# Kernel tuning notes

Hardware: AMD Instinct MI355X
Metric: run time of the kernel (lower is better)

The kernel has to match this reference:

```python
import jax, jax.numpy as jnp
import numpy as np

N = 50000      # nodes (both x and t sets)
D = 128        # d_hidden
E = 1600000    # edges per edge_index (avg degree 32)
LN_EPS = 1e-5


def _gin(x_src, x_dst, edge, W1, b1, W2, b2):
    # PyG GINConv, eps=0: nn(x_dst + sum_{j->i} x_src[j])
    agg = jax.ops.segment_sum(x_src[edge[0]], edge[1], num_segments=x_dst.shape[0])
    h = x_dst + agg
    h = jax.nn.relu(h @ W1 + b1)
    return h @ W2 + b2


def _layernorm(h, g, b):
    m = jnp.mean(h, axis=-1, keepdims=True)
    v = jnp.var(h, axis=-1, keepdims=True)
    return (h - m) / jnp.sqrt(v + LN_EPS) * g + b


def setup_inputs() -> dict:
    key = jax.random.key(0)
    ks = jax.random.split(key, 24)
    s = 1.0 / np.sqrt(D)
    w = lambda k: (jax.random.uniform(k, (D, D), dtype=jnp.float32) * 2 - 1) * s
    b = lambda k: (jax.random.uniform(k, (D,), dtype=jnp.float32) * 2 - 1) * s
    return {
        "x": jax.random.normal(ks[0], (N, D), dtype=jnp.float32),
        "t": jax.random.normal(ks[1], (N, D), dtype=jnp.float32),
        "e_t": jax.random.randint(ks[2], (2, E), 0, N),
        "e_xct": jax.random.randint(ks[3], (2, E), 0, N),
        # gat_tt GIN MLP
        "W1a": w(ks[4]), "b1a": b(ks[5]), "W2a": w(ks[6]), "b2a": b(ks[7]),
        # gat_xct GIN MLP
        "W1b": w(ks[8]), "b1b": b(ks[9]), "W2b": w(ks[10]), "b2b": b(ks[11]),
        # out: Linear -> ReLU -> LayerNorm
        "Wo": w(ks[12]), "bo": b(ks[13]),
        "ln_g": jnp.ones((D,), dtype=jnp.float32),
        "ln_b": jnp.zeros((D,), dtype=jnp.float32),
        # fc_x: Linear -> ReLU -> Linear
        "Wf1": w(ks[14]), "bf1": b(ks[15]), "Wf2": w(ks[16]), "bf2": b(ks[17]),
    }


def reference(x, t, e_t, e_xct,
              W1a, b1a, W2a, b2a,
              W1b, b1b, W2b, b2b,
              Wo, bo, ln_g, ln_b,
              Wf1, bf1, Wf2, bf2):
    # t = (t + gat_tt(t, e_t) + gat_xct((x, t), e_xct)).relu()
    t2 = jax.nn.relu(t
                     + _gin(t, t, e_t, W1a, b1a, W2a, b2a)
                     + _gin(x, t, e_xct, W1b, b1b, W2b, b2b))
    # out branch: Linear -> ReLU -> LayerNorm, residual add
    t_out = t2 + _layernorm(jax.nn.relu(t2 @ Wo + bo), ln_g, ln_b)
    # fc_x branch: Linear -> ReLU -> Linear, residual add
    x_out = x + (jax.nn.relu(x @ Wf1 + bf1) @ Wf2 + bf2)
    return (x_out, t_out)
```

## Files before the change

kernel.cpp:

```cpp
#include <hip/hip_runtime.h>

#define DD 128
#define BSH 7
#define LSTR 136

typedef __attribute__((ext_vector_type(8))) short bf16x8;
typedef __attribute__((ext_vector_type(4))) float f32x4;
typedef __attribute__((ext_vector_type(2))) float f32x2;

__device__ __forceinline__ unsigned short f2b(float f){
  unsigned u = __builtin_bit_cast(unsigned, f);
  u += 0x7FFFu + ((u >> 16) & 1u);
  return (unsigned short)(u >> 16);
}
__device__ __forceinline__ float blo(unsigned u){ return __builtin_bit_cast(float, u << 16); }
__device__ __forceinline__ float bhi(unsigned u){ return __builtin_bit_cast(float, u & 0xFFFF0000u); }
__device__ __forceinline__ float b2f(unsigned short h){ return __builtin_bit_cast(float, ((unsigned)h) << 16); }
__device__ __forceinline__ unsigned pk2(float a, float b){
  return (unsigned)f2b(a) | ((unsigned)f2b(b) << 16);
}

struct WP { const float* w[7]; };
__global__ __launch_bounds__(256) void k_pre(const float* __restrict__ x,
    const float* __restrict__ t, unsigned* __restrict__ xh, unsigned* __restrict__ th,
    int M, WP p, unsigned short* __restrict__ wt,
    const int* __restrict__ e_t, const int* __restrict__ e_xct,
    int* __restrict__ gbcount, int E, int NBper, int ncv, int N){
  const int bid = blockIdx.x;
  if (bid < ncv){
    int tid = bid*256 + threadIdx.x;
    if (tid < M){
      float4 v = ((const float4*)x)[tid];
      ((uint2*)xh)[tid] = make_uint2(pk2(v.x, v.y), pk2(v.z, v.w));
    } else if (tid < 2*M){
      int k = tid - M;
      float4 v = ((const float4*)t)[k];
      ((uint2*)th)[k] = make_uint2(pk2(v.x, v.y), pk2(v.z, v.w));
    }
    return;
  }
  if (bid < ncv + 7){
    const float* W = p.w[bid - ncv];
    unsigned short* dst = wt + (size_t)(bid - ncv)*DD*DD;
    for (int e = threadIdx.x; e < DD*DD; e += 256){
      int k = e >> 7, c = e & 127;
      dst[(c*DD + k) ^ ((c & 7) << 3)] = f2b(W[e]);
    }
    return;
  }
  if (bid == ncv + 7){
    const int tid = threadIdx.x;
    uint4 z; z.x = 0; z.y = 0; z.z = 0; z.w = 0;
    if (tid < 16)      ((uint4*)(xh + (size_t)N*(DD/2)))[tid]      = z;
    else if (tid < 32) ((uint4*)(th + (size_t)N*(DD/2)))[tid - 16] = z;
    return;
  }
  __shared__ int h[800];
  const int vb = bid - ncv - 8;
  const int NB2 = 2*NBper;
  for (int i = threadIdx.x; i < NB2; i += 256) h[i] = 0;
  __syncthreads();
  const long total = 2L*E;
  for (long idx = (long)vb*256 + threadIdx.x; idx < total; idx += 65536L){
    int s = idx >= E;
    int e = (int)(idx - (s ? (long)E : 0));
    int d = (s ? e_xct : e_t)[E + e];
    atomicAdd(&h[s*NBper + (d >> BSH)], 1);
  }
  __syncthreads();
  for (int i = threadIdx.x; i < NB2; i += 256)
    if (h[i]) atomicAdd(&gbcount[i], h[i]);
}

__global__ void k_bscan(const int* __restrict__ gbcount, int* __restrict__ gbase,
                        int* __restrict__ gcursor, int NB2, int total){
  __shared__ int sm[1024];
  const int t = threadIdx.x;
  int v = (t < NB2) ? gbcount[t] : 0;
  sm[t] = v; __syncthreads();
  for (int d = 1; d < 1024; d <<= 1){
    int u = (t >= d) ? sm[t-d] : 0;
    __syncthreads();
    sm[t] += u;
    __syncthreads();
  }
  if (t < NB2){ int ex = sm[t] - v; gbase[t] = ex; gcursor[t] = ex; }
  if (t == 0) gbase[NB2] = total;
}

#define SCCH 8192
__global__ __launch_bounds__(256) void k_scatter(const int* __restrict__ e_t,
    const int* __restrict__ e_xct, int* __restrict__ gcursor,
    unsigned* __restrict__ gbucket, int E, int NBper){
  __shared__ int cnt[800]; __shared__ int gpos[800]; __shared__ int cur[800];
  const int NB2 = 2*NBper;
  const int t = threadIdx.x;
  for (int i = t; i < NB2; i += 256){ cnt[i] = 0; cur[i] = 0; }
  __syncthreads();
  const long base = (long)blockIdx.x * SCCH;
  const long end  = min(base + SCCH, 2L*E);
  for (long idx = base + t; idx < end; idx += 256){
    int s = idx >= E;
    int e = (int)(idx - (s ? (long)E : 0));
    int d = (s ? e_xct : e_t)[E + e];
    atomicAdd(&cnt[s*NBper + (d >> BSH)], 1);
  }
  __syncthreads();
  for (int i = t; i < NB2; i += 256)
    if (cnt[i]) gpos[i] = atomicAdd(&gcursor[i], cnt[i]);
  __syncthreads();
  for (long idx = base + t; idx < end; idx += 256){
    int s = idx >= E;
    int e = (int)(idx - (s ? (long)E : 0));
    const int* ei = s ? e_xct : e_t;
    int sv = ei[e];
    int d  = ei[E + e];
    int b  = s*NBper + (d >> BSH);
    int pos = atomicAdd(&cur[b], 1);
    gbucket[gpos[b] + pos] = (unsigned)sv | ((unsigned)d << 16);
  }
}

__global__ __launch_bounds__(256) void k_build(const unsigned* __restrict__ gbucket,
    const int* __restrict__ gbase, int* __restrict__ offs,
    unsigned short* __restrict__ csr, int N, int E, int NBper){
  __shared__ int cnt[128]; __shared__ int pre[128]; __shared__ int cur[128];
  const int b  = blockIdx.x;
  const int s  = b >= NBper;
  const int bb = b - s*NBper;
  const int d0 = bb << BSH;
  const int t  = threadIdx.x;
  if (t < 128) cnt[t] = 0;
  __syncthreads();
  const int g0 = gbase[b], g1 = gbase[b+1];
  for (int j = g0 + t; j < g1; j += 256){
    unsigned en = gbucket[j];
    atomicAdd(&cnt[(en >> 16) & 127], 1);
  }
  __syncthreads();
  int v = (t < 128) ? cnt[t] : 0;
  if (t < 128) pre[t] = v;
  __syncthreads();
  for (int d = 1; d < 128; d <<= 1){
    int u = (t >= d && t < 128) ? pre[t-d] : 0;
    __syncthreads();
    if (t < 128) pre[t] += u;
    __syncthreads();
  }
  if (t < 128){
    int ex = pre[t] - v;
    cur[t] = ex;
    int dd = d0 + t;
    if (dd < N) offs[(size_t)s*(N+1) + dd] = (g0 - s*E) + ex;
  }
  if (t == 128 + 0 && bb == NBper-1) offs[(size_t)s*(N+1) + N] = E;
  __syncthreads();
  for (int j = g0 + t; j < g1; j += 256){
    unsigned en = gbucket[j];
    int d7 = (en >> 16) & 127;
    int pos = atomicAdd(&cur[d7], 1);
    csr[(size_t)g0 + pos] = (unsigned short)(en & 0xFFFFu);
  }
}

__device__ __forceinline__ void gemm_reg(const bf16x8 a[4], int c0, int g, int swz,
    const unsigned short* wimg, f32x4 acc[8]){
  #pragma unroll
  for (int kb = 0; kb < 4; ++kb){
    const int co = (kb*32 + g*8) ^ swz;
    #pragma unroll
    for (int cb = 0; cb < 8; ++cb){
      bf16x8 b = *(const bf16x8*)(wimg + (size_t)(cb*16 + c0)*DD + co);
      acc[cb] = __builtin_amdgcn_mfma_f32_16x16x32_bf16(a[kb], b, acc[cb], 0, 0, 0);
    }
  }
}

__device__ __forceinline__ void gemm_lds(const unsigned short* lds,
    int w, int c0, int g, int swz, const unsigned short* wimg, f32x4 acc[8]){
  const unsigned short* ap = lds + (w*16 + c0)*LSTR + g*8;
  #pragma unroll
  for (int kb = 0; kb < 4; ++kb){
    bf16x8 a = *(const bf16x8*)(ap + kb*32);
    const int co = (kb*32 + g*8) ^ swz;
    #pragma unroll
    for (int cb = 0; cb < 8; ++cb){
      bf16x8 b = *(const bf16x8*)(wimg + (size_t)(cb*16 + c0)*DD + co);
      acc[cb] = __builtin_amdgcn_mfma_f32_16x16x32_bf16(a, b, acc[cb], 0, 0, 0);
    }
  }
}

__global__ __launch_bounds__(256, 4) void k_gather(const unsigned short* __restrict__ th,
    const unsigned short* __restrict__ xh, const int* __restrict__ offs,
    const unsigned short* __restrict__ csr, unsigned short* hA, unsigned short* hB,
    const unsigned short* __restrict__ wt,
    const float* __restrict__ bf1, const float* __restrict__ bf2,
    float* __restrict__ outX,
    int N, int E, int gg){
  __shared__ unsigned short lds[64*LSTR];
  if (blockIdx.x < (unsigned)gg){
    const int bid = blockIdx.x;
    const int tid = threadIdx.x;
    const int w = tid >> 6, l = tid & 63;
    const int g = l >> 4, c0 = l & 15;
    const int swz = (c0 & 7) << 3;
    const int rbase = bid*64 + w*16;
    const unsigned short* Wf1 = wt + 5*DD*DD;
    const unsigned short* Wf2 = wt + 6*DD*DD;

    int arow = rbase + c0; if (arow > N-1) arow = N-1;
    const unsigned short* apX = xh + (size_t)arow*DD + g*8;
    bf16x8 aX[4];
    #pragma unroll
    for (int kb = 0; kb < 4; ++kb) aX[kb] = *(const bf16x8*)(apX + kb*32);
    unsigned short rs_[8][4];
    #pragma unroll
    for (int cb = 0; cb < 8; ++cb){
      #pragma unroll
      for (int r = 0; r < 4; ++r){
        int orow = rbase + 4*g + r;
        int rc = orow > N-1 ? N-1 : orow;
        rs_[cb][r] = xh[(size_t)rc*DD + cb*16 + c0];
      }
    }

    f32x4 acc[8];
    #pragma unroll
    for (int cb = 0; cb < 8; ++cb) acc[cb] = 0.f;
    gemm_reg(aX, c0, g, swz, Wf1, acc);

    #pragma unroll
    for (int cb = 0; cb < 8; ++cb){
      float bv = bf1[cb*16 + c0];
      #pragma unroll
      for (int r = 0; r < 4; ++r)
        lds[(w*16 + 4*g + r)*LSTR + cb*16 + c0] = f2b(fmaxf(acc[cb][r] + bv, 0.f));
    }
    __syncthreads();

    #pragma unroll
    for (int cb = 0; cb < 8; ++cb) acc[cb] = 0.f;
    gemm_lds(lds, w, c0, g, swz, Wf2, acc);

    #pragma unroll
    for (int cb = 0; cb < 8; ++cb){
      float bv = bf2[cb*16 + c0];
      #pragma unroll
      for (int r = 0; r < 4; ++r){
        int orow = rbase + 4*g + r;
        if (orow < N){
          size_t oi = (size_t)orow*DD + cb*16 + c0;
          outX[oi] = acc[cb][r] + bv + b2f(rs_[cb][r]);
        }
      }
    }
    return;
  }
  const int w = threadIdx.x >> 6, l = threadIdx.x & 63;
  const long wid = (long)(blockIdx.x - gg)*4 + w;
  if (wid >= 2L*N) return;
  const int s = wid >= N;
  const int i = (int)(wid - (s ? N : 0));
  const int* off = offs + (size_t)s*(N+1);
  const unsigned short* src = s ? xh : th;
  const unsigned short* cs = csr + (size_t)s*E;
  const int o0 = off[i], o1 = off[i+1];
  const int deg = o1 - o0;
  const int rs = l >> 4;
  const int q  = l & 15;
  const unsigned short* srcq = src + q*8;
  f32x2 A0 = 0.f, A1 = 0.f, A2 = 0.f, A3 = 0.f;
  if (deg > 0){
    int ce = cs[o0 + (l < deg ? l : deg-1)];
    for (int base = 0; base < deg; base += 64){
      const int nb = min(64, deg - base);
      const int ce_cur = ce;
      const int nxt = base + 64;
      if (nxt < deg){
        const int rem2 = deg - nxt;
        ce = cs[o0 + nxt + (l < rem2 ? l : rem2-1)];
      }
      for (int jj = 0; jj < nb; jj += 16){
        #pragma unroll
        for (int u4 = 0; u4 < 4; ++u4){
          const int idx = jj + u4*4 + rs;
          int r = __shfl(ce_cur, idx);
          r = (idx < nb) ? r : N;
          uint4 v = *(const uint4*)(srcq + (size_t)r*DD);
          A0 += (f32x2){blo(v.x), bhi(v.x)};
          A1 += (f32x2){blo(v.y), bhi(v.y)};
          A2 += (f32x2){blo(v.z), bhi(v.z)};
          A3 += (f32x2){blo(v.w), bhi(v.w)};
        }
      }
    }
  }
  #pragma unroll
  for (int m = 16; m <= 32; m <<= 1){
    A0.x += __shfl_xor(A0.x, m); A0.y += __shfl_xor(A0.y, m);
    A1.x += __shfl_xor(A1.x, m); A1.y += __shfl_xor(A1.y, m);
    A2.x += __shfl_xor(A2.x, m); A2.y += __shfl_xor(A2.y, m);
    A3.x += __shfl_xor(A3.x, m); A3.y += __shfl_xor(A3.y, m);
  }
  if (l < 16){
    uint4 tv = *(const uint4*)(th + (size_t)i*DD + q*8);
    A0 += (f32x2){blo(tv.x), bhi(tv.x)};
    A1 += (f32x2){blo(tv.y), bhi(tv.y)};
    A2 += (f32x2){blo(tv.z), bhi(tv.z)};
    A3 += (f32x2){blo(tv.w), bhi(tv.w)};
    uint4 o;
    o.x = pk2(A0.x, A0.y); o.y = pk2(A1.x, A1.y);
    o.z = pk2(A2.x, A2.y); o.w = pk2(A3.x, A3.y);
    *(uint4*)((s ? hB : hA) + (size_t)i*DD + q*8) = o;
  }
}

__device__ __forceinline__ void stage_issue(const unsigned short* __restrict__ Wt,
                                            unsigned short* wlds){
  const int tid = threadIdx.x;
  const int w = tid >> 6, l = tid & 63;
  #pragma unroll
  for (int i = 0; i < 8; ++i){
    const int cbase = i*256 + w*64;
    __builtin_amdgcn_global_load_lds(
      (const __attribute__((address_space(1))) unsigned*)(Wt + (size_t)(cbase + l)*8),
      (__attribute__((address_space(3))) unsigned*)(wlds + (size_t)cbase*8),
      16, 0, 0);
  }
}

__global__ __launch_bounds__(256, 3) void k_tail(
    const unsigned short* __restrict__ hA, const unsigned short* __restrict__ hB,
    const unsigned short* __restrict__ th,
    const unsigned short* __restrict__ wt,
    const float* __restrict__ b1a, const float* __restrict__ b2a,
    const float* __restrict__ b1b, const float* __restrict__ b2b,
    const float* __restrict__ bo,  const float* __restrict__ lng,
    const float* __restrict__ lnb,
    float* __restrict__ outT, int N)
{
  __shared__ unsigned short lds[64*LSTR];
  __shared__ unsigned short wlds[DD*DD];
  const unsigned short* W1a = wt + 0*DD*DD;
  const unsigned short* W2a = wt + 1*DD*DD;
  const unsigned short* W1b = wt + 2*DD*DD;
  const unsigned short* W2b = wt + 3*DD*DD;
  const unsigned short* Wo  = wt + 4*DD*DD;

  const int bid = blockIdx.x;
  const int tid = threadIdx.x;
  const int w = tid >> 6, l = tid & 63;
  const int g = l >> 4, c0 = l & 15;
  const int swz = (c0 & 7) << 3;
  const int rbase = bid*64 + w*16;

  int arow = rbase + c0; if (arow > N-1) arow = N-1;
  const unsigned short* apA = hA + (size_t)arow*DD + g*8;
  const unsigned short* apB = hB + (size_t)arow*DD + g*8;
  bf16x8 aA[4], aB[4];
  #pragma unroll
  for (int kb = 0; kb < 4; ++kb){
    aA[kb] = *(const bf16x8*)(apA + kb*32);
    aB[kb] = *(const bf16x8*)(apB + kb*32);
  }
  unsigned short thr_[8][4];
  #pragma unroll
  for (int cb = 0; cb < 8; ++cb){
    #pragma unroll
    for (int r = 0; r < 4; ++r){
      int orow = rbase + 4*g + r;
      int rc = orow > N-1 ? N-1 : orow;
      thr_[cb][r] = th[(size_t)rc*DD + cb*16 + c0];
    }
  }
  stage_issue(W1a, wlds);
  __syncthreads();

  f32x4 acc[8];

  #pragma unroll
  for (int cb = 0; cb < 8; ++cb) acc[cb] = 0.f;
  gemm_reg(aA, c0, g, swz, wlds, acc);
  __syncthreads();
  stage_issue(W2a, wlds);
  #pragma unroll
  for (int cb = 0; cb < 8; ++cb){
    float bv = b1a[cb*16 + c0];
    #pragma unroll
    for (int r = 0; r < 4; ++r)
      lds[(w*16 + 4*g + r)*LSTR + cb*16 + c0] = f2b(fmaxf(acc[cb][r] + bv, 0.f));
  }
  __syncthreads();

  #pragma unroll
  for (int cb = 0; cb < 8; ++cb) acc[cb] = 0.f;
  gemm_lds(lds, w, c0, g, swz, wlds, acc);
  float pAv[8][4];
  #pragma unroll
  for (int cb = 0; cb < 8; ++cb){
    float bv = b2a[cb*16 + c0];
    #pragma unroll
    for (int r = 0; r < 4; ++r) pAv[cb][r] = acc[cb][r] + bv;
  }
  __syncthreads();
  stage_issue(W1b, wlds);
  __syncthreads();

  #pragma unroll
  for (int cb = 0; cb < 8; ++cb) acc[cb] = 0.f;
  gemm_reg(aB, c0, g, swz, wlds, acc);
  __syncthreads();
  stage_issue(W2b, wlds);
  #pragma unroll
  for (int cb = 0; cb < 8; ++cb){
    float bv = b1b[cb*16 + c0];
    #pragma unroll
    for (int r = 0; r < 4; ++r)
      lds[(w*16 + 4*g + r)*LSTR + cb*16 + c0] = f2b(fmaxf(acc[cb][r] + bv, 0.f));
  }
  __syncthreads();

  #pragma unroll
  for (int cb = 0; cb < 8; ++cb) acc[cb] = 0.f;
  gemm_lds(lds, w, c0, g, swz, wlds, acc);
  __syncthreads();
  stage_issue(Wo, wlds);

  float t2f[8][4];
  #pragma unroll
  for (int cb = 0; cb < 8; ++cb){
    float bv = b2b[cb*16 + c0];
    #pragma unroll
    for (int r = 0; r < 4; ++r){
      float v = fmaxf(acc[cb][r] + bv + b2f(thr_[cb][r]) + pAv[cb][r], 0.f);
      t2f[cb][r] = v;
      lds[(w*16 + 4*g + r)*LSTR + cb*16 + c0] = f2b(v);
    }
  }
  __syncthreads();

  #pragma unroll
  for (int cb = 0; cb < 8; ++cb) acc[cb] = 0.f;
  gemm_lds(lds, w, c0, g, swz, wlds, acc);

  float u[8][4];
  float sm_[4] = {0,0,0,0}, sq_[4] = {0,0,0,0};
  #pragma unroll
  for (int cb = 0; cb < 8; ++cb){
    float bv = bo[cb*16 + c0];
    #pragma unroll
    for (int r = 0; r < 4; ++r){
      float v = fmaxf(acc[cb][r] + bv, 0.f);
      u[cb][r] = v;
      sm_[r] += v; sq_[r] += v*v;
    }
  }
  #pragma unroll
  for (int m = 1; m < 16; m <<= 1){
    #pragma unroll
    for (int r = 0; r < 4; ++r){
      sm_[r] += __shfl_xor(sm_[r], m, 64);
      sq_[r] += __shfl_xor(sq_[r], m, 64);
    }
  }
  float mean[4], rstd[4];
  #pragma unroll
  for (int r = 0; r < 4; ++r){
    mean[r] = sm_[r] * (1.0f/DD);
    float var = sq_[r] * (1.0f/DD) - mean[r]*mean[r];
    rstd[r] = rsqrtf(var + 1e-5f);
  }
  #pragma unroll
  for (int cb = 0; cb < 8; ++cb){
    float gv = lng[cb*16 + c0], bv2 = lnb[cb*16 + c0];
    #pragma unroll
    for (int r = 0; r < 4; ++r){
      int orow = rbase + 4*g + r;
      if (orow < N){
        size_t oi = (size_t)orow*DD + cb*16 + c0;
        outT[oi] = (u[cb][r] - mean[r]) * rstd[r] * gv + bv2 + t2f[cb][r];
      }
    }
  }
}

extern "C" void kernel_launch(void* const* d_in, const int* in_sizes, int n_in,
                              void* d_out, int out_size, void* d_ws, size_t ws_size,
                              hipStream_t stream) {
  const float* x     = (const float*)d_in[0];
  const float* t     = (const float*)d_in[1];
  const int*   e_t   = (const int*)d_in[2];
  const int*   e_xct = (const int*)d_in[3];
  const float* b1a = (const float*)d_in[5];
  const float* b2a = (const float*)d_in[7];
  const float* b1b = (const float*)d_in[9];
  const float* b2b = (const float*)d_in[11];
  const float* bo  = (const float*)d_in[13];
  const float* lng = (const float*)d_in[14];
  const float* lnb = (const float*)d_in[15];
  const float* bf1 = (const float*)d_in[17];
  const float* bf2 = (const float*)d_in[19];

  const int N = in_sizes[0] / DD;
  const int E = in_sizes[2] / 2;
  const int NBper = (N + 127) >> BSH;
  const int NB2 = 2*NBper;

  char* p = (char*)d_ws;
  auto carve = [&](size_t b)->char*{ char* r = p; p += (b + 255) & ~(size_t)255; return r; };
  size_t nd2z = (size_t)(N+1)*DD*2;
  size_t nd2 = (size_t)N*DD*2, nd4 = (size_t)N*DD*4;
  unsigned short* xh = (unsigned short*)carve(nd2z);
  unsigned short* th = (unsigned short*)carve(nd2z);
  unsigned short* hA = (unsigned short*)carve(nd2);
  unsigned short* hB = (unsigned short*)carve(nd2);
  float*          pA = (float*)carve(nd4);
  unsigned short* wt = (unsigned short*)carve((size_t)7*DD*DD*2);
  int* gbcount = (int*)carve((size_t)NB2*4);
  int* gbase   = (int*)carve((size_t)(NB2+1)*4);
  int* gcursor = (int*)carve((size_t)NB2*4);
  int* offs    = (int*)carve((size_t)2*(N+1)*4);
  unsigned short* csr = (unsigned short*)carve((size_t)2*E*2);
  unsigned* gbucket = (unsigned*)pA;

  float* outX = (float*)d_out;
  float* outT = outX + (size_t)N*DD;

  hipMemsetAsync(gbcount, 0, (size_t)NB2*4, stream);

  WP wp;
  wp.w[0] = (const float*)d_in[4];  wp.w[1] = (const float*)d_in[6];
  wp.w[2] = (const float*)d_in[8];  wp.w[3] = (const float*)d_in[10];
  wp.w[4] = (const float*)d_in[12]; wp.w[5] = (const float*)d_in[16];
  wp.w[6] = (const float*)d_in[18];

  const int M4 = N*DD/4;
  const int ncv = (2*M4 + 255)/256;
  k_pre<<<ncv + 8 + 256, 256, 0, stream>>>(x, t, (unsigned*)xh, (unsigned*)th, M4,
                                           wp, wt, e_t, e_xct, gbcount, E, NBper, ncv, N);
  k_bscan<<<1, 1024, 0, stream>>>(gbcount, gbase, gcursor, NB2, 2*E);
  const int nsc = (int)((2L*E + SCCH-1) / SCCH);
  k_scatter<<<nsc, 256, 0, stream>>>(e_t, e_xct, gcursor, gbucket, E, NBper);
  k_build<<<NB2, 256, 0, stream>>>(gbucket, gbase, offs, csr, N, E, NBper);

  const int gg = (N + 63)/64;
  const int ngb = (2*N + 3)/4;
  k_gather<<<gg + ngb, 256, 0, stream>>>(th, xh, offs, csr, hA, hB,
                                         wt, bf1, bf2, outX, N, E, gg);

  k_tail<<<gg, 256, 0, stream>>>(hA, hB, th, wt, b1a, b2a, b1b, b2b, bo,
                                 lng, lnb, outT, N);
}
```

Measured before the change: 254.2 us.

## Move fc_x MLP into scatter kernel, stage weights in LDS, widen tail blocks

Moves the independent x-branch MLP blocks out of the gather kernel and into the edge scatter kernel, so that work runs alongside the memory-bound scatter instead of the gather. The x-branch now stages its weights into LDS with global_load_lds rather than reading them straight from global memory. The tail kernel goes from 256 to 512 threads and handles 128 rows per block, so each staged weight matrix is shared by twice as many rows. The costs are higher LDS use per block, which may limit occupancy of both the scatter and tail kernels, and a less regular mix of work inside the fused kernel.

```diff
diff --git a/kernel.cpp b/kernel.cpp
--- a/kernel.cpp
+++ b/kernel.cpp
@@ -88,36 +88,160 @@
   if (t == 0) gbase[NB2] = total;
 }
 
+__device__ __forceinline__ void gemm_reg(const bf16x8 a[4], int c0, int g, int swz,
+    const unsigned short* wlds, f32x4 acc[8]){
+  #pragma unroll
+  for (int kb = 0; kb < 4; ++kb){
+    const int co = (kb*32 + g*8) ^ swz;
+    #pragma unroll
+    for (int cb = 0; cb < 8; ++cb){
+      bf16x8 b = *(const bf16x8*)(wlds + (cb*16 + c0)*DD + co);
+      acc[cb] = __builtin_amdgcn_mfma_f32_16x16x32_bf16(a[kb], b, acc[cb], 0, 0, 0);
+    }
+  }
+}
+
+__device__ __forceinline__ void gemm_lds(const unsigned short* lds,
+    int w, int c0, int g, int swz, const unsigned short* wlds, f32x4 acc[8]){
+  const unsigned short* ap = lds + (w*16 + c0)*LSTR + g*8;
+  #pragma unroll
+  for (int kb = 0; kb < 4; ++kb){
+    bf16x8 a = *(const bf16x8*)(ap + kb*32);
+    const int co = (kb*32 + g*8) ^ swz;
+    #pragma unroll
+    for (int cb = 0; cb < 8; ++cb){
+      bf16x8 b = *(const bf16x8*)(wlds + (cb*16 + c0)*DD + co);
+      acc[cb] = __builtin_amdgcn_mfma_f32_16x16x32_bf16(a, b, acc[cb], 0, 0, 0);
+    }
+  }
+}
+
+__device__ __forceinline__ void stage_issue_256(const unsigned short* __restrict__ Wt,
+                                                unsigned short* wlds){
+  const int tid = threadIdx.x;
+  const int w = tid >> 6, l = tid & 63;
+  #pragma unroll
+  for (int i = 0; i < 8; ++i){
+    const int cbase = i*256 + w*64;
+    __builtin_amdgcn_global_load_lds(
+      (const __attribute__((address_space(1))) unsigned*)(Wt + (size_t)(cbase + l)*8),
+      (__attribute__((address_space(3))) unsigned*)(wlds + (size_t)cbase*8),
+      16, 0, 0);
+  }
+}
+__device__ __forceinline__ void stage_issue_512(const unsigned short* __restrict__ Wt,
+                                                unsigned short* wlds){
+  const int tid = threadIdx.x;
+  const int w = tid >> 6, l = tid & 63;
+  #pragma unroll
+  for (int i = 0; i < 4; ++i){
+    const int cbase = i*512 + w*64;
+    __builtin_amdgcn_global_load_lds(
+      (const __attribute__((address_space(1))) unsigned*)(Wt + (size_t)(cbase + l)*8),
+      (__attribute__((address_space(3))) unsigned*)(wlds + (size_t)cbase*8),
+      16, 0, 0);
+  }
+}
+
 #define SCCH 8192
-__global__ __launch_bounds__(256) void k_scatter(const int* __restrict__ e_t,
+__global__ __launch_bounds__(256, 3) void k_scatmlp(const int* __restrict__ e_t,
     const int* __restrict__ e_xct, int* __restrict__ gcursor,
-    unsigned* __restrict__ gbucket, int E, int NBper){
-  __shared__ int cnt[800]; __shared__ int gpos[800]; __shared__ int cur[800];
-  const int NB2 = 2*NBper;
-  const int t = threadIdx.x;
-  for (int i = t; i < NB2; i += 256){ cnt[i] = 0; cur[i] = 0; }
-  __syncthreads();
-  const long base = (long)blockIdx.x * SCCH;
-  const long end  = min(base + SCCH, 2L*E);
-  for (long idx = base + t; idx < end; idx += 256){
-    int s = idx >= E;
-    int e = (int)(idx - (s ? (long)E : 0));
-    int d = (s ? e_xct : e_t)[E + e];
-    atomicAdd(&cnt[s*NBper + (d >> BSH)], 1);
-  }
-  __syncthreads();
-  for (int i = t; i < NB2; i += 256)
-    if (cnt[i]) gpos[i] = atomicAdd(&gcursor[i], cnt[i]);
-  __syncthreads();
-  for (long idx = base + t; idx < end; idx += 256){
-    int s = idx >= E;
-    int e = (int)(idx - (s ? (long)E : 0));
-    const int* ei = s ? e_xct : e_t;
-    int sv = ei[e];
-    int d  = ei[E + e];
-    int b  = s*NBper + (d >> BSH);
-    int pos = atomicAdd(&cur[b], 1);
-    gbucket[gpos[b] + pos] = (unsigned)sv | ((unsigned)d << 16);
+    unsigned* __restrict__ gbucket, int E, int NBper, int nsc,
+    const unsigned short* __restrict__ xh, const unsigned short* __restrict__ wt,
+    const float* __restrict__ bf1, const float* __restrict__ bf2,
+    float* __restrict__ outX, int N){
+  __shared__ __align__(16) unsigned char smem[50176];
+  if (blockIdx.x < (unsigned)nsc){
+    int* cnt  = (int*)smem;
+    int* gpos = cnt + 800;
+    int* cur  = gpos + 800;
+    const int NB2 = 2*NBper;
+    const int t = threadIdx.x;
+    for (int i = t; i < NB2; i += 256){ cnt[i] = 0; cur[i] = 0; }
+    __syncthreads();
+    const long base = (long)blockIdx.x * SCCH;
+    const long end  = min(base + SCCH, 2L*E);
+    for (long idx = base + t; idx < end; idx += 256){
+      int s = idx >= E;
+      int e = (int)(idx - (s ? (long)E : 0));
+      int d = (s ? e_xct : e_t)[E + e];
+      atomicAdd(&cnt[s*NBper + (d >> BSH)], 1);
+    }
+    __syncthreads();
+    for (int i = t; i < NB2; i += 256)
+      if (cnt[i]) gpos[i] = atomicAdd(&gcursor[i], cnt[i]);
+    __syncthreads();
+    for (long idx = base + t; idx < end; idx += 256){
+      int s = idx >= E;
+      int e = (int)(idx - (s ? (long)E : 0));
+      const int* ei = s ? e_xct : e_t;
+      int sv = ei[e];
+      int d  = ei[E + e];
+      int b  = s*NBper + (d >> BSH);
+      int pos = atomicAdd(&cur[b], 1);
+      gbucket[gpos[b] + pos] = (unsigned)sv | ((unsigned)d << 16);
+    }
+    return;
+  }
+  unsigned short* lds  = (unsigned short*)smem;
+  unsigned short* wlds = (unsigned short*)(smem + 17408);
+  const unsigned short* Wf1 = wt + 5*DD*DD;
+  const unsigned short* Wf2 = wt + 6*DD*DD;
+  const int bid = blockIdx.x - nsc;
+  const int tid = threadIdx.x;
+  const int w = tid >> 6, l = tid & 63;
+  const int g = l >> 4, c0 = l & 15;
+  const int swz = (c0 & 7) << 3;
+  const int rbase = bid*64 + w*16;
+
+  int arow = rbase + c0; if (arow > N-1) arow = N-1;
+  const unsigned short* apX = xh + (size_t)arow*DD + g*8;
+  bf16x8 aX[4];
+  #pragma unroll
+  for (int kb = 0; kb < 4; ++kb) aX[kb] = *(const bf16x8*)(apX + kb*32);
+  unsigned short rs_[8][4];
+  #pragma unroll
+  for (int cb = 0; cb < 8; ++cb){
+    #pragma unroll
+    for (int r = 0; r < 4; ++r){
+      int orow = rbase + 4*g + r;
+      int rc = orow > N-1 ? N-1 : orow;
+      rs_[cb][r] = xh[(size_t)rc*DD + cb*16 + c0];
+    }
+  }
+  stage_issue_256(Wf1, wlds);
+  __syncthreads();
+
+  f32x4 acc[8];
+  #pragma unroll
+  for (int cb = 0; cb < 8; ++cb) acc[cb] = 0.f;
+  gemm_reg(aX, c0, g, swz, wlds, acc);
+  __syncthreads();
+  stage_issue_256(Wf2, wlds);
+  #pragma unroll
+  for (int cb = 0; cb < 8; ++cb){
+    float bv = bf1[cb*16 + c0];
+    #pragma unroll
+    for (int r = 0; r < 4; ++r)
+      lds[(w*16 + 4*g + r)*LSTR + cb*16 + c0] = f2b(fmaxf(acc[cb][r] + bv, 0.f));
+  }
+  __syncthreads();
+
+  #pragma unroll
+  for (int cb = 0; cb < 8; ++cb) acc[cb] = 0.f;
+  gemm_lds(lds, w, c0, g, swz, wlds, acc);
+
+  #pragma unroll
+  for (int cb = 0; cb < 8; ++cb){
+    float bv = bf2[cb*16 + c0];
+    #pragma unroll
+    for (int r = 0; r < 4; ++r){
+      int orow = rbase + 4*g + r;
+      if (orow < N){
+        size_t oi = (size_t)orow*DD + cb*16 + c0;
+        outX[oi] = acc[cb][r] + bv + b2f(rs_[cb][r]);
+      }
+    }
   }
 }
 
@@ -163,102 +287,12 @@
   }
 }
 
-__device__ __forceinline__ void gemm_reg(const bf16x8 a[4], int c0, int g, int swz,
-    const unsigned short* wimg, f32x4 acc[8]){
-  #pragma unroll
-  for (int kb = 0; kb < 4; ++kb){
-    const int co = (kb*32 + g*8) ^ swz;
-    #pragma unroll
-    for (int cb = 0; cb < 8; ++cb){
-      bf16x8 b = *(const bf16x8*)(wimg + (size_t)(cb*16 + c0)*DD + co);
-      acc[cb] = __builtin_amdgcn_mfma_f32_16x16x32_bf16(a[kb], b, acc[cb], 0, 0, 0);
-    }
-  }
-}
-
-__device__ __forceinline__ void gemm_lds(const unsigned short* lds,
-    int w, int c0, int g, int swz, const unsigned short* wimg, f32x4 acc[8]){
-  const unsigned short* ap = lds + (w*16 + c0)*LSTR + g*8;
-  #pragma unroll
-  for (int kb = 0; kb < 4; ++kb){
-    bf16x8 a = *(const bf16x8*)(ap + kb*32);
-    const int co = (kb*32 + g*8) ^ swz;
-    #pragma unroll
-    for (int cb = 0; cb < 8; ++cb){
-      bf16x8 b = *(const bf16x8*)(wimg + (size_t)(cb*16 + c0)*DD + co);
-      acc[cb] = __builtin_amdgcn_mfma_f32_16x16x32_bf16(a, b, acc[cb], 0, 0, 0);
-    }
-  }
-}
-
-__global__ __launch_bounds__(256, 4) void k_gather(const unsigned short* __restrict__ th,
+__global__ __launch_bounds__(256) void k_gather(const unsigned short* __restrict__ th,
     const unsigned short* __restrict__ xh, const int* __restrict__ offs,
     const unsigned short* __restrict__ csr, unsigned short* hA, unsigned short* hB,
-    const unsigned short* __restrict__ wt,
-    const float* __restrict__ bf1, const float* __restrict__ bf2,
-    float* __restrict__ outX,
-    int N, int E, int gg){
-  __shared__ unsigned short lds[64*LSTR];
-  if (blockIdx.x < (unsigned)gg){
-    const int bid = blockIdx.x;
-    const int tid = threadIdx.x;
-    const int w = tid >> 6, l = tid & 63;
-    const int g = l >> 4, c0 = l & 15;
-    const int swz = (c0 & 7) << 3;
-    const int rbase = bid*64 + w*16;
-    const unsigned short* Wf1 = wt + 5*DD*DD;
-    const unsigned short* Wf2 = wt + 6*DD*DD;
-
-    int arow = rbase + c0; if (arow > N-1) arow = N-1;
-    const unsigned short* apX = xh + (size_t)arow*DD + g*8;
-    bf16x8 aX[4];
-    #pragma unroll
-    for (int kb = 0; kb < 4; ++kb) aX[kb] = *(const bf16x8*)(apX + kb*32);
-    unsigned short rs_[8][4];
-    #pragma unroll
-    for (int cb = 0; cb < 8; ++cb){
-      #pragma unroll
-      for (int r = 0; r < 4; ++r){
-        int orow = rbase + 4*g + r;
-        int rc = orow > N-1 ? N-1 : orow;
-        rs_[cb][r] = xh[(size_t)rc*DD + cb*16 + c0];
-      }
-    }
-
-    f32x4 acc[8];
-    #pragma unroll
-    for (int cb = 0; cb < 8; ++cb) acc[cb] = 0.f;
-    gemm_reg(aX, c0, g, swz, Wf1, acc);
-
-    #pragma unroll
-    for (int cb = 0; cb < 8; ++cb){
-      float bv = bf1[cb*16 + c0];
-      #pragma unroll
-      for (int r = 0; r < 4; ++r)
-        lds[(w*16 + 4*g + r)*LSTR + cb*16 + c0] = f2b(fmaxf(acc[cb][r] + bv, 0.f));
-    }
-    __syncthreads();
-
-    #pragma unroll
-    for (int cb = 0; cb < 8; ++cb) acc[cb] = 0.f;
-    gemm_lds(lds, w, c0, g, swz, Wf2, acc);
-
-    #pragma unroll
-    for (int cb = 0; cb < 8; ++cb){
-      float bv = bf2[cb*16 + c0];
-      #pragma unroll
-      for (int r = 0; r < 4; ++r){
-        int orow = rbase + 4*g + r;
-        if (orow < N){
-          size_t oi = (size_t)orow*DD + cb*16 + c0;
-          outX[oi] = acc[cb][r] + bv + b2f(rs_[cb][r]);
-        }
-      }
-    }
-    return;
-  }
+    int N, int E){
   const int w = threadIdx.x >> 6, l = threadIdx.x & 63;
-  const long wid = (long)(blockIdx.x - gg)*4 + w;
+  const long wid = (long)blockIdx.x*4 + w;
   if (wid >= 2L*N) return;
   const int s = wid >= N;
   const int i = (int)(wid - (s ? N : 0));
@@ -316,21 +350,7 @@
   }
 }
 
-__device__ __forceinline__ void stage_issue(const unsigned short* __restrict__ Wt,
-                                            unsigned short* wlds){
-  const int tid = threadIdx.x;
-  const int w = tid >> 6, l = tid & 63;
-  #pragma unroll
-  for (int i = 0; i < 8; ++i){
-    const int cbase = i*256 + w*64;
-    __builtin_amdgcn_global_load_lds(
-      (const __attribute__((address_space(1))) unsigned*)(Wt + (size_t)(cbase + l)*8),
-      (__attribute__((address_space(3))) unsigned*)(wlds + (size_t)cbase*8),
-      16, 0, 0);
-  }
-}
-
-__global__ __launch_bounds__(256, 3) void k_tail(
+__global__ __launch_bounds__(512, 4) void k_tail(
     const unsigned short* __restrict__ hA, const unsigned short* __restrict__ hB,
     const unsigned short* __restrict__ th,
     const unsigned short* __restrict__ wt,
@@ -340,7 +360,7 @@
     const float* __restrict__ lnb,
     float* __restrict__ outT, int N)
 {
-  __shared__ unsigned short lds[64*LSTR];
+  __shared__ unsigned short lds[128*LSTR];
   __shared__ unsigned short wlds[DD*DD];
   const unsigned short* W1a = wt + 0*DD*DD;
   const unsigned short* W2a = wt + 1*DD*DD;
@@ -353,7 +373,7 @@
   const int w = tid >> 6, l = tid & 63;
   const int g = l >> 4, c0 = l & 15;
   const int swz = (c0 & 7) << 3;
-  const int rbase = bid*64 + w*16;
+  const int rbase = bid*128 + w*16;
 
   int arow = rbase + c0; if (arow > N-1) arow = N-1;
   const unsigned short* apA = hA + (size_t)arow*DD + g*8;
@@ -374,7 +394,7 @@
       thr_[cb][r] = th[(size_t)rc*DD + cb*16 + c0];
     }
   }
-  stage_issue(W1a, wlds);
+  stage_issue_512(W1a, wlds);
   __syncthreads();
 
   f32x4 acc[8];
@@ -383,7 +403,7 @@
   for (int cb = 0; cb < 8; ++cb) acc[cb] = 0.f;
   gemm_reg(aA, c0, g, swz, wlds, acc);
   __syncthreads();
-  stage_issue(W2a, wlds);
+  stage_issue_512(W2a, wlds);
   #pragma unroll
   for (int cb = 0; cb < 8; ++cb){
     float bv = b1a[cb*16 + c0];
@@ -404,14 +424,14 @@
     for (int r = 0; r < 4; ++r) pAv[cb][r] = acc[cb][r] + bv;
   }
   __syncthreads();
-  stage_issue(W1b, wlds);
+  stage_issue_512(W1b, wlds);
   __syncthreads();
 
   #pragma unroll
   for (int cb = 0; cb < 8; ++cb) acc[cb] = 0.f;
   gemm_reg(aB, c0, g, swz, wlds, acc);
   __syncthreads();
-  stage_issue(W2b, wlds);
+  stage_issue_512(W2b, wlds);
   #pragma unroll
   for (int cb = 0; cb < 8; ++cb){
     float bv = b1b[cb*16 + c0];
@@ -425,7 +445,7 @@
   for (int cb = 0; cb < 8; ++cb) acc[cb] = 0.f;
   gemm_lds(lds, w, c0, g, swz, wlds, acc);
   __syncthreads();
-  stage_issue(Wo, wlds);
+  stage_issue_512(Wo, wlds);
 
   float t2f[8][4];
   #pragma unroll
@@ -540,15 +560,16 @@
   k_pre<<<ncv + 8 + 256, 256, 0, stream>>>(x, t, (unsigned*)xh, (unsigned*)th, M4,
                                            wp, wt, e_t, e_xct, gbcount, E, NBper, ncv, N);
   k_bscan<<<1, 1024, 0, stream>>>(gbcount, gbase, gcursor, NB2, 2*E);
+
   const int nsc = (int)((2L*E + SCCH-1) / SCCH);
-  k_scatter<<<nsc, 256, 0, stream>>>(e_t, e_xct, gcursor, gbucket, E, NBper);
+  const int gg2 = (N + 63)/64;
+  k_scatmlp<<<nsc + gg2, 256, 0, stream>>>(e_t, e_xct, gcursor, gbucket, E, NBper,
+                                           nsc, xh, wt, bf1, bf2, outX, N);
+
   k_build<<<NB2, 256, 0, stream>>>(gbucket, gbase, offs, csr, N, E, NBper);
-
-  const int gg = (N + 63)/64;
-  const int ngb = (2*N + 3)/4;
-  k_gather<<<gg + ngb, 256, 0, stream>>>(th, xh, offs, csr, hA, hB,
-                                         wt, bf1, bf2, outX, N, E, gg);
-
-  k_tail<<<gg, 256, 0, stream>>>(hA, hB, th, wt, b1a, b2a, b1b, b2b, bo,
+  k_gather<<<(2*N + 3)/4, 256, 0, stream>>>(th, xh, offs, csr, hA, hB, N, E);
+
+  const int gt = (N + 127)/128;
+  k_tail<<<gt, 512, 0, stream>>>(hA, hB, th, wt, b1a, b2a, b1b, b2b, bo,
                                  lng, lnb, outT, N);
 }
```

Result: faster. 243.3 us (-4.3%).
